# Performance work log

Measured on AMD Instinct MI355X. Metric: run time of the kernel, lower is better.

The kernel has to match this reference:

```python
import jax, jax.numpy as jnp
import numpy as np
import math

N_SRC = 100000
N_DST0 = 30000
N_DST1 = 8000
E0 = 200000
E1 = 80000
H, D = 4, 64


def gat_conv(h_src, h_dst, src, dst, W, al, ar, b, n_dst):
    """DGL GATConv (allow_zero_in_degree=True): shared fc, LeakyReLU(0.2), edge softmax."""
    z_src = (h_src @ W).reshape(-1, H, D)              # [Ns,H,D]
    z_dst = (h_dst @ W).reshape(-1, H, D)              # [Nd,H,D]
    el = jnp.sum(z_src * al, axis=-1)                  # [Ns,H]
    er = jnp.sum(z_dst * ar, axis=-1)                  # [Nd,H]
    e = jax.nn.leaky_relu(el[src] + er[dst], 0.2)      # [E,H]
    emax = jax.ops.segment_max(e, dst, num_segments=n_dst)
    emax = jnp.where(jnp.isfinite(emax), emax, 0.0)
    ex = jnp.exp(e - emax[dst])
    denom = jax.ops.segment_sum(ex, dst, num_segments=n_dst)
    denom = jnp.where(denom > 0, denom, 1.0)
    alpha = ex / denom[dst]                            # [E,H]
    out = jax.ops.segment_sum(alpha[:, :, None] * z_src[src], dst, num_segments=n_dst)
    return out + b.reshape(1, H, D)                    # [Nd,H,D]


def attn_pool(feat):
    """Self attention over relation/head slots, then mean over slots (attention(f,f,f).mean(dim=1))."""
    d = feat.shape[-1]
    scores = jnp.einsum('nsd,ntd->nst', feat, feat) / math.sqrt(d)
    p = jax.nn.softmax(scores, axis=-1)
    out = jnp.einsum('nst,ntd->nsd', p, feat)
    return out.mean(axis=1)                            # [N,d]


def rgat_layer(xu, xi, eii, eiu, eui, W, al, ar, b, n_dst_u, n_dst_i):
    du, di = xu[:n_dst_u], xi[:n_dst_i]
    # sorted canonical etypes: ('item','ii','item') < ('item','iu','user') < ('user','ui','item')
    out_ii = gat_conv(xi, di, eii[0], eii[1], W[0], al[0], ar[0], b[0], n_dst_i)
    out_iu = gat_conv(xi, du, eiu[0], eiu[1], W[1], al[1], ar[1], b[1], n_dst_u)
    out_ui = gat_conv(xu, di, eui[0], eui[1], W[2], al[2], ar[2], b[2], n_dst_i)
    feat_u = out_iu                                    # [Nu, H, D]
    feat_i = jnp.concatenate([out_ii, out_ui], axis=1) # [Ni, 2H, D]
    hu = attn_pool(feat_u)
    hi = attn_pool(feat_i)
    return jnp.concatenate([du, hu], axis=1), jnp.concatenate([di, hi], axis=1)


def setup_inputs() -> dict:
    key = jax.random.key(0)
    ks = jax.random.split(key, 24)
    inp = {
        'x_user': jax.random.normal(ks[0], (N_SRC, 64), jnp.float32),
        'x_item': jax.random.normal(ks[1], (N_SRC, 64), jnp.float32),
        'e0_ii_src': jax.random.randint(ks[2], (E0,), 0, N_SRC, jnp.int32),
        'e0_ii_dst': jax.random.randint(ks[3], (E0,), 0, N_DST0, jnp.int32),
        'e0_iu_src': jax.random.randint(ks[4], (E0,), 0, N_SRC, jnp.int32),
        'e0_iu_dst': jax.random.randint(ks[5], (E0,), 0, N_DST0, jnp.int32),
        'e0_ui_src': jax.random.randint(ks[6], (E0,), 0, N_SRC, jnp.int32),
        'e0_ui_dst': jax.random.randint(ks[7], (E0,), 0, N_DST0, jnp.int32),
        'e1_ii_src': jax.random.randint(ks[8], (E1,), 0, N_DST0, jnp.int32),
        'e1_ii_dst': jax.random.randint(ks[9], (E1,), 0, N_DST1, jnp.int32),
        'e1_iu_src': jax.random.randint(ks[10], (E1,), 0, N_DST0, jnp.int32),
        'e1_iu_dst': jax.random.randint(ks[11], (E1,), 0, N_DST1, jnp.int32),
        'e1_ui_src': jax.random.randint(ks[12], (E1,), 0, N_DST0, jnp.int32),
        'e1_ui_dst': jax.random.randint(ks[13], (E1,), 0, N_DST1, jnp.int32),
        'W0': jax.random.normal(ks[14], (3, 64, H * D), jnp.float32) * 0.1,
        'al0': jax.random.normal(ks[15], (3, H, D), jnp.float32) * 0.1,
        'ar0': jax.random.normal(ks[16], (3, H, D), jnp.float32) * 0.1,
        'b0': jnp.zeros((3, H * D), jnp.float32),
        'W1': jax.random.normal(ks[17], (3, 128, H * D), jnp.float32) * 0.1,
        'al1': jax.random.normal(ks[18], (3, H, D), jnp.float32) * 0.1,
        'ar1': jax.random.normal(ks[19], (3, H, D), jnp.float32) * 0.1,
        'b1': jnp.zeros((3, H * D), jnp.float32),
    }
    return inp


def reference(x_user, x_item,
              e0_ii_src, e0_ii_dst, e0_iu_src, e0_iu_dst, e0_ui_src, e0_ui_dst,
              e1_ii_src, e1_ii_dst, e1_iu_src, e1_iu_dst, e1_ui_src, e1_ui_dst,
              W0, al0, ar0, b0, W1, al1, ar1, b1):
    xu, xi = rgat_layer(x_user, x_item,
                        (e0_ii_src, e0_ii_dst), (e0_iu_src, e0_iu_dst), (e0_ui_src, e0_ui_dst),
                        W0, al0, ar0, b0, N_DST0, N_DST0)
    xu, xi = rgat_layer(xu, xi,
                        (e1_ii_src, e1_ii_dst), (e1_iu_src, e1_iu_dst), (e1_ui_src, e1_ui_dst),
                        W1, al1, ar1, b1, N_DST1, N_DST1)
    return jnp.concatenate([xu, xi], axis=0)  # [2*N_DST1, 128+64]
```

## Files before the change

### kernel.cpp

```cpp
#include <hip/hip_runtime.h>

#define NSRC   100000
#define NDST0  30000
#define NDST1  8000
#define E0N    200000
#define E1N    80000
#define HD     256
#define DD     64
#define CAPB   32

typedef short bf16x8 __attribute__((ext_vector_type(8)));
typedef float f32x4  __attribute__((ext_vector_type(4)));

static __device__ __forceinline__ unsigned short f2bf(float f) {
    unsigned u = __float_as_uint(f);
    u += 0x7fffu + ((u >> 16) & 1u);
    return (unsigned short)(u >> 16);
}
static __device__ __forceinline__ unsigned pack2(float a, float b) {
    return (unsigned)f2bf(a) | ((unsigned)f2bf(b) << 16);
}
static __device__ __forceinline__ void fma4(float4& a, float s, const float4& b) {
    a.x = fmaf(s, b.x, a.x); a.y = fmaf(s, b.y, a.y);
    a.z = fmaf(s, b.z, a.z); a.w = fmaf(s, b.w, a.w);
}
static __device__ __forceinline__ float dot4(const float4& a, const float4& b) {
    return fmaf(a.x, b.x, fmaf(a.y, b.y, fmaf(a.z, b.z, a.w * b.w)));
}
static __device__ __forceinline__ float4 ld_bf4(const unsigned short* p) {
    uint2 u = *reinterpret_cast<const uint2*>(p);
    float4 r;
    r.x = __uint_as_float(u.x << 16);
    r.y = __uint_as_float(u.x & 0xffff0000u);
    r.z = __uint_as_float(u.y << 16);
    r.w = __uint_as_float(u.y & 0xffff0000u);
    return r;
}

static __device__ void wlr_prep(const float* __restrict__ W, const float* __restrict__ al,
                                const float* __restrict__ ar, float* __restrict__ wl,
                                float* __restrict__ wr, int K, int tid)
{
    int r = tid / (K * 4);
    int rem = tid - r * K * 4;
    int k = rem >> 2, h = rem & 3;
    const float* wrow = W + (size_t)r * K * HD + (size_t)k * HD + h * DD;
    const float* a_l = al + r * HD + h * DD;
    const float* a_r = ar + r * HD + h * DD;
    float sl = 0.f, sr = 0.f;
    for (int d = 0; d < DD; ++d) {
        float w = wrow[d];
        sl = fmaf(w, a_l[d], sl);
        sr = fmaf(w, a_r[d], sr);
    }
    wl[r * 512 + k * 4 + h] = sl;
    wr[r * 512 + k * 4 + h] = sr;
}
static __device__ void wt_prep(const float* __restrict__ W, unsigned short* __restrict__ Wt,
                               int K, int r, int c)
{
    const float* Wr = W + (size_t)r * K * HD;
    unsigned short* Wtr = Wt + (size_t)r * 256 * K;
    for (int k = 0; k < K; k += 2) {
        float a = Wr[(size_t)k * HD + c];
        float b = Wr[(size_t)(k + 1) * HD + c];
        *reinterpret_cast<unsigned*>(Wtr + (size_t)c * K + k) = pack2(a, b);
    }
}
static __device__ void fill_aos(const int* __restrict__ ed, const int* __restrict__ es,
                                int* __restrict__ cnt, int* __restrict__ bsrc,
                                int E, int nd, int r, int e)
{
    if (e >= E) return;
    int d = __builtin_nontemporal_load(ed + e);
    int c = atomicAdd(&cnt[(size_t)r * nd + d], 1);
    if (c < CAPB) {
        int s = __builtin_nontemporal_load(es + e);
        __builtin_nontemporal_store(s, &bsrc[((size_t)r * nd + d) * CAPB + c]);
    }
}
template<int K>
static __device__ void prep_row(bool item, int row, int nd,
                                const float* __restrict__ XA, const float* __restrict__ XB,
                                const float* __restrict__ wl3, const float* __restrict__ wr3,
                                float* __restrict__ el3, float* __restrict__ er3)
{
    const float* X = item ? XA : XB;
    const float4* xv = reinterpret_cast<const float4*>(X + (size_t)row * K);
    const float4* wlAv = reinterpret_cast<const float4*>(item ? wl3 : wl3 + 1024);
    const float4* wlBv = reinterpret_cast<const float4*>(wl3 + 512);
    float4 aA = make_float4(0.f, 0.f, 0.f, 0.f), aB = aA;
    #pragma unroll 4
    for (int c = 0; c < K / 4; ++c) {
        float4 x4 = xv[c];
        fma4(aA, x4.x, wlAv[c * 4 + 0]); fma4(aA, x4.y, wlAv[c * 4 + 1]);
        fma4(aA, x4.z, wlAv[c * 4 + 2]); fma4(aA, x4.w, wlAv[c * 4 + 3]);
        if (item) {
            fma4(aB, x4.x, wlBv[c * 4 + 0]); fma4(aB, x4.y, wlBv[c * 4 + 1]);
            fma4(aB, x4.z, wlBv[c * 4 + 2]); fma4(aB, x4.w, wlBv[c * 4 + 3]);
        }
    }
    if (item) {
        *reinterpret_cast<float4*>(el3 + (size_t)row * 4) = aA;
        *reinterpret_cast<float4*>(el3 + (size_t)NSRC * 4 + (size_t)row * 4) = aB;
    } else {
        *reinterpret_cast<float4*>(el3 + (size_t)2 * NSRC * 4 + (size_t)row * 4) = aA;
    }
    if (row < nd) {
        const float4* wrAv = reinterpret_cast<const float4*>(item ? wr3 : wr3 + 512);
        const float4* wrBv = reinterpret_cast<const float4*>(wr3 + 1024);
        float4 rA = make_float4(0.f, 0.f, 0.f, 0.f), rB = rA;
        #pragma unroll 4
        for (int c = 0; c < K / 4; ++c) {
            float4 x4 = xv[c];
            fma4(rA, x4.x, wrAv[c * 4 + 0]); fma4(rA, x4.y, wrAv[c * 4 + 1]);
            fma4(rA, x4.z, wrAv[c * 4 + 2]); fma4(rA, x4.w, wrAv[c * 4 + 3]);
            if (item) {
                fma4(rB, x4.x, wrBv[c * 4 + 0]); fma4(rB, x4.y, wrBv[c * 4 + 1]);
                fma4(rB, x4.z, wrBv[c * 4 + 2]); fma4(rB, x4.w, wrBv[c * 4 + 3]);
            }
        }
        if (item) {
            *reinterpret_cast<float4*>(er3 + (size_t)row * 4) = rA;
            *reinterpret_cast<float4*>(er3 + (size_t)2 * NDST0 * 4 + (size_t)row * 4) = rB;
        } else {
            *reinterpret_cast<float4*>(er3 + (size_t)NDST0 * 4 + (size_t)row * 4) = rA;
        }
    }
}
template<int S>
static __device__ void pool_node(const unsigned short* __restrict__ srcA, const float* __restrict__ bA,
                                 const unsigned short* __restrict__ srcB, const float* __restrict__ bB,
                                 const float* __restrict__ base, int baseCols,
                                 float* __restrict__ dst, int pitch, int colOff,
                                 int node, int q)
{
    float4 f[S];
    #pragma unroll
    for (int s = 0; s < S; ++s) {
        const unsigned short* sp = (s < 4) ? (srcA + (size_t)node * HD + s * DD)
                                           : (srcB + (size_t)node * HD + (s - 4) * DD);
        const float* bp = (s < 4) ? (bA + s * DD) : (bB + (s - 4) * DD);
        float4 v = ld_bf4(sp + q * 4);
        float4 b = *reinterpret_cast<const float4*>(bp + q * 4);
        v.x += b.x; v.y += b.y; v.z += b.z; v.w += b.w;
        f[s] = v;
    }
    constexpr int NE = S * (S + 1) / 2;
    float gt[NE];
    {
        int idx = 0;
        #pragma unroll
        for (int s = 0; s < S; ++s)
            #pragma unroll
            for (int t = s; t < S; ++t)
                gt[idx++] = dot4(f[s], f[t]);
    }
    #pragma unroll
    for (int m = 1; m < 16; m <<= 1) {
        #pragma unroll
        for (int i = 0; i < NE; ++i) gt[i] += __shfl_xor(gt[i], m, 16);
    }
    auto Gv = [&](int s, int t) -> float {
        int a = s < t ? s : t, b2 = s < t ? t : s;
        return gt[a * S - a * (a - 1) / 2 + (b2 - a)];
    };
    float g[S];
    #pragma unroll
    for (int t = 0; t < S; ++t) g[t] = 0.f;
    #pragma unroll
    for (int s = 0; s < S; ++s) {
        float sc[S];
        float m = -1e30f;
        #pragma unroll
        for (int t = 0; t < S; ++t) { sc[t] = Gv(s, t) * 0.125f; m = sc[t] > m ? sc[t] : m; }
        float pe[S];
        float sum = 0.f;
        #pragma unroll
        for (int t = 0; t < S; ++t) { pe[t] = __expf(sc[t] - m); sum += pe[t]; }
        float inv = 1.f / sum;
        #pragma unroll
        for (int t = 0; t < S; ++t) g[t] += pe[t] * inv;
    }
    float4 o = make_float4(0.f, 0.f, 0.f, 0.f);
    #pragma unroll
    for (int t = 0; t < S; ++t) fma4(o, g[t], f[t]);
    const float is = 1.f / S;
    o.x *= is; o.y *= is; o.z *= is; o.w *= is;
    *reinterpret_cast<float4*>(dst + (size_t)node * pitch + colOff + q * 4) = o;
    for (int c = q * 4; c < baseCols; c += 64) {
        float4 v = *reinterpret_cast<const float4*>(base + (size_t)node * baseCols + c);
        *reinterpret_cast<float4*>(dst + (size_t)node * pitch + c) = v;
    }
}

__global__ void k_wsetup(const float* W0, const float* al0, const float* ar0,
                         const float* W1, const float* al1, const float* ar1,
                         float* wlA, float* wrA, unsigned short* WtA,
                         float* wlB, float* wrB, unsigned short* WtB,
                         int* cntA, int* cntB)
{
    int bx = blockIdx.x, t = threadIdx.x;
    if (bx < 3)       { wlr_prep(W0, al0, ar0, wlA, wrA, 64,  bx * 256 + t); return; }
    if (bx < 9)       { wlr_prep(W1, al1, ar1, wlB, wrB, 128, (bx - 3) * 256 + t); return; }
    if (bx < 12)      { wt_prep(W0, WtA, 64,  bx - 9,  t); return; }
    if (bx < 15)      { wt_prep(W1, WtB, 128, bx - 12, t); return; }
    bx -= 15;
    if (bx < 88) {
        int i = bx * 256 + t;
        if (i < 22500) reinterpret_cast<int4*>(cntA)[i] = make_int4(0, 0, 0, 0);
        return;
    }
    bx -= 88;
    {
        int i = bx * 256 + t;
        if (i < 6000) reinterpret_cast<int4*>(cntB)[i] = make_int4(0, 0, 0, 0);
    }
}

__global__ __launch_bounds__(256, 4) void k_prepfill(
    const float* x_item, const float* x_user,
    const float* wlA, const float* wrA,
    float* el3, float* er3,
    const int* ed0, const int* ed1, const int* ed2,
    const int* es0, const int* es1, const int* es2,
    const int* ed3, const int* ed4, const int* ed5,
    const int* es3, const int* es4, const int* es5,
    int* cntA, int* bsrcA, int* cntB, int* bsrcB,
    int bprP, int bpr0, int bpr1)
{
    int bx = blockIdx.x;
    int t = threadIdx.x;
    if (bx < 2 * bprP) {
        const bool item = bx < bprP;
        int row = (item ? bx : bx - bprP) * 256 + t;
        if (row < NSRC)
            prep_row<64>(item, row, NDST0, x_item, x_user, wlA, wrA, el3, er3);
        return;
    }
    bx -= 2 * bprP;
    if (bx < 3 * bpr0) {
        int r = (bx >= 2 * bpr0) ? 2 : (bx >= bpr0 ? 1 : 0);
        int e = (bx - r * bpr0) * 256 + t;
        const int* ed = (r == 0) ? ed0 : (r == 1 ? ed1 : ed2);
        const int* es = (r == 0) ? es0 : (r == 1 ? es1 : es2);
        fill_aos(ed, es, cntA, bsrcA, E0N, NDST0, r, e);
        return;
    }
    bx -= 3 * bpr0;
    {
        int r = (bx >= 2 * bpr1) ? 2 : (bx >= bpr1 ? 1 : 0);
        int e = (bx - r * bpr1) * 256 + t;
        const int* ed = (r == 0) ? ed3 : (r == 1 ? ed4 : ed5);
        const int* es = (r == 0) ? es3 : (r == 1 ? es4 : es5);
        fill_aos(ed, es, cntB, bsrcB, E1N, NDST1, r, e);
    }
}

template<int K>
__global__ __launch_bounds__(256) void k_prep_x2(const float* __restrict__ XA,
                                                 const float* __restrict__ XB,
                                                 int M, int nd, int bpr,
                                                 const float* __restrict__ wl3,
                                                 const float* __restrict__ wr3,
                                                 float* __restrict__ el3,
                                                 float* __restrict__ er3)
{
    int bx = blockIdx.x;
    const bool item = bx < bpr;
    int row = (item ? bx : bx - bpr) * 256 + threadIdx.x;
    if (row >= M) return;
    prep_row<K>(item, row, nd, XA, XB, wl3, wr3, el3, er3);
}

template<int K>
__global__ __launch_bounds__(256) void k_agg3(const int* __restrict__ cnt,
                                              const int* __restrict__ bsrc,
                                              const float* __restrict__ el3,
                                              const float* __restrict__ er3,
                                              const float* __restrict__ xsA,
                                              const float* __restrict__ xsB,
                                              unsigned short* __restrict__ aggX,
                                              int nd, int bpr)
{
    constexpr int NV = K / 64;
    __shared__ float exs[4][64][8];
    int bx = blockIdx.x;
    int r = (bx >= 2 * bpr) ? 2 : (bx >= bpr ? 1 : 0);
    int wid = ((bx - r * bpr) * 256 + (int)threadIdx.x) >> 6;
    int lane = threadIdx.x & 63;
    if (wid >= nd) return;
    int q = lane & 15, g = lane >> 4, w = threadIdx.x >> 6;
    const float* el = el3 + (size_t)r * NSRC * 4;
    const float* xsrc = (r < 2) ? xsA : xsB;
    int c = cnt[(size_t)r * nd + wid]; if (c > CAPB) c = CAPB;
    const int* lst = bsrc + ((size_t)r * nd + wid) * CAPB;
    float4 er4 = *reinterpret_cast<const float4*>(er3 + (size_t)r * NDST0 * 4 + (size_t)wid * 4);

    if (lane < c) {
        int s = lst[lane];
        float4 e4 = *reinterpret_cast<const float4*>(el + (size_t)s * 4);
        e4.x += er4.x; e4.y += er4.y; e4.z += er4.z; e4.w += er4.w;
        e4.x = e4.x > 0.f ? e4.x : 0.2f * e4.x;
        e4.y = e4.y > 0.f ? e4.y : 0.2f * e4.y;
        e4.z = e4.z > 0.f ? e4.z : 0.2f * e4.z;
        e4.w = e4.w > 0.f ? e4.w : 0.2f * e4.w;
        float sF = __int_as_float(s);
        float4 h0 = make_float4(sF, __expf(e4.x), sF, __expf(e4.y));
        float4 h1 = make_float4(sF, __expf(e4.z), sF, __expf(e4.w));
        *reinterpret_cast<float4*>(&exs[w][lane][0]) = h0;
        *reinterpret_cast<float4*>(&exs[w][lane][4]) = h1;
    }

    float4 acc[NV];
    #pragma unroll
    for (int v = 0; v < NV; ++v) acc[v] = make_float4(0.f, 0.f, 0.f, 0.f);
    float den = 0.f;
    const char* xb = reinterpret_cast<const char*>(xsrc) + q * (NV * 16);

    for (int b0 = 0; b0 < c; b0 += 4) {
        const int n = c - b0;
        float2 se0, se1, se2, se3;
        float4 x0[NV], x1[NV], x2[NV], x3[NV];
        se0 = *reinterpret_cast<const float2*>(&exs[w][b0][g * 2]);
        {
            const float4* xp = reinterpret_cast<const float4*>(
                xb + (size_t)((unsigned)__float_as_int(se0.x) * (K * 4)));
            #pragma unroll
            for (int v = 0; v < NV; ++v) x0[v] = xp[v];
        }
        if (n > 1) {
            se1 = *reinterpret_cast<const float2*>(&exs[w][b0 + 1][g * 2]);
            const float4* xp = reinterpret_cast<const float4*>(
                xb + (size_t)((unsigned)__float_as_int(se1.x) * (K * 4)));
            #pragma unroll
            for (int v = 0; v < NV; ++v) x1[v] = xp[v];
        }
        if (n > 2) {
            se2 = *reinterpret_cast<const float2*>(&exs[w][b0 + 2][g * 2]);
            const float4* xp = reinterpret_cast<const float4*>(
                xb + (size_t)((unsigned)__float_as_int(se2.x) * (K * 4)));
            #pragma unroll
            for (int v = 0; v < NV; ++v) x2[v] = xp[v];
        }
        if (n > 3) {
            se3 = *reinterpret_cast<const float2*>(&exs[w][b0 + 3][g * 2]);
            const float4* xp = reinterpret_cast<const float4*>(
                xb + (size_t)((unsigned)__float_as_int(se3.x) * (K * 4)));
            #pragma unroll
            for (int v = 0; v < NV; ++v) x3[v] = xp[v];
        }
        den += se0.y;
        #pragma unroll
        for (int v = 0; v < NV; ++v) fma4(acc[v], se0.y, x0[v]);
        if (n > 1) {
            den += se1.y;
            #pragma unroll
            for (int v = 0; v < NV; ++v) fma4(acc[v], se1.y, x1[v]);
        }
        if (n > 2) {
            den += se2.y;
            #pragma unroll
            for (int v = 0; v < NV; ++v) fma4(acc[v], se2.y, x2[v]);
        }
        if (n > 3) {
            den += se3.y;
            #pragma unroll
            for (int v = 0; v < NV; ++v) fma4(acc[v], se3.y, x3[v]);
        }
    }
    float inv = den > 0.f ? 1.f / den : 0.f;
    unsigned short* op = aggX + (((size_t)r * nd + wid) * 4 + g) * K + q * 4 * NV;
    if (NV == 1) {
        uint2 wv;
        wv.x = pack2(acc[0].x * inv, acc[0].y * inv);
        wv.y = pack2(acc[0].z * inv, acc[0].w * inv);
        *reinterpret_cast<uint2*>(op) = wv;
    } else {
        uint4 wv;
        wv.x = pack2(acc[0].x * inv, acc[0].y * inv);
        wv.y = pack2(acc[0].z * inv, acc[0].w * inv);
        wv.z = pack2(acc[1].x * inv, acc[1].y * inv);
        wv.w = pack2(acc[1].z * inv, acc[1].w * inv);
        *reinterpret_cast<uint4*>(op) = wv;
    }
}

template<int K>
__global__ __launch_bounds__(256) void k_gemm3(const unsigned short* __restrict__ aggX,
                                               const unsigned short* __restrict__ Wt3,
                                               unsigned short* __restrict__ outb,
                                               int nd, int bpr)
{
    int bx = blockIdx.x;
    int r = (bx >= 2 * bpr) ? 2 : (bx >= bpr ? 1 : 0);
    const unsigned short* A  = aggX + (size_t)r * nd * 4 * K;
    const unsigned short* Wt = Wt3 + (size_t)r * 256 * K;
    unsigned short* ob = outb + (size_t)r * NDST0 * HD;
    const int lane = threadIdx.x & 63;
    const int wv = threadIdx.x >> 6;
    const int r0 = (bx - r * bpr) * 16;
    const int rr = lane & 15, kg = lane >> 4;
    f32x4 acc[4] = {{0.f,0.f,0.f,0.f},{0.f,0.f,0.f,0.f},{0.f,0.f,0.f,0.f},{0.f,0.f,0.f,0.f}};
    const unsigned short* ap = A + ((size_t)(r0 + rr) * 4 + wv) * K + kg * 8;
    #pragma unroll
    for (int kb = 0; kb < K; kb += 32) {
        bf16x8 a = *reinterpret_cast<const bf16x8*>(ap + kb);
        #pragma unroll
        for (int n = 0; n < 4; ++n) {
            const unsigned short* wp = Wt + (size_t)(wv * 64 + n * 16 + rr) * K + kb + kg * 8;
            bf16x8 b = *reinterpret_cast<const bf16x8*>(wp);
            acc[n] = __builtin_amdgcn_mfma_f32_16x16x32_bf16(a, b, acc[n], 0, 0, 0);
        }
    }
    #pragma unroll
    for (int n = 0; n < 4; ++n)
        #pragma unroll
        for (int i = 0; i < 4; ++i)
            ob[(size_t)(r0 + kg * 4 + i) * HD + wv * 64 + n * 16 + rr] = f2bf(acc[n][i]);
}

__global__ __launch_bounds__(256) void k_pools(
    const unsigned short* pA4, const float* bA4, const unsigned short* pB4, const float* bB4,
    const float* base4, int cols4, float* dst4, int pitch4, int off4,
    const unsigned short* pA8, const float* bA8, const unsigned short* pB8, const float* bB8,
    const float* base8, int cols8, float* dst8, int pitch8, int off8,
    int n, int bp)
{
    int bx = blockIdx.x;
    int t = threadIdx.x;
    const bool four = bx < bp;
    int bl = four ? bx : bx - bp;
    int node = ((bl * 256 + t) >> 6) * 4 + ((t & 63) >> 4);
    int q = t & 15;
    if (node >= n) return;
    if (four) pool_node<4>(pA4, bA4, pB4, bB4, base4, cols4, dst4, pitch4, off4, node, q);
    else      pool_node<8>(pA8, bA8, pB8, bB8, base8, cols8, dst8, pitch8, off8, node, q);
}

extern "C" void kernel_launch(void* const* d_in, const int* in_sizes, int n_in,
                              void* d_out, int out_size, void* d_ws, size_t ws_size,
                              hipStream_t stream)
{
    const float* x_user = (const float*)d_in[0];
    const float* x_item = (const float*)d_in[1];
    const int* e_s[6] = { (const int*)d_in[2], (const int*)d_in[4], (const int*)d_in[6],
                          (const int*)d_in[8], (const int*)d_in[10], (const int*)d_in[12] };
    const int* e_d[6] = { (const int*)d_in[3], (const int*)d_in[5], (const int*)d_in[7],
                          (const int*)d_in[9], (const int*)d_in[11], (const int*)d_in[13] };
    const float* W0  = (const float*)d_in[14];
    const float* al0 = (const float*)d_in[15];
    const float* ar0 = (const float*)d_in[16];
    const float* b0  = (const float*)d_in[17];
    const float* W1  = (const float*)d_in[18];
    const float* al1 = (const float*)d_in[19];
    const float* ar1 = (const float*)d_in[20];
    const float* b1  = (const float*)d_in[21];
    float* out = (float*)d_out;
    (void)in_sizes; (void)n_in; (void)out_size; (void)ws_size;

    char* p = (char*)d_ws;
    auto take = [&](size_t bytes) { char* r = p; p += (bytes + 255) & ~(size_t)255; return r; };
    unsigned short* out3 = (unsigned short*)take((size_t)3 * NDST0 * HD * 2);
    float* xu1  = (float*)take((size_t)NDST0 * 128 * 4);
    float* xi1  = (float*)take((size_t)NDST0 * 128 * 4);
    unsigned short* aggX = (unsigned short*)take((size_t)3 * NDST0 * 4 * DD * 2);
    float* el3  = (float*)take((size_t)3 * NSRC * 4 * 4);
    float* er3  = (float*)take((size_t)3 * NDST0 * 4 * 4);
    int*   cntA = (int*)take((size_t)3 * NDST0 * 4);
    int*   cntB = (int*)take((size_t)3 * NDST1 * 4);
    int*   bsrcA = (int*)take((size_t)3 * NDST0 * CAPB * 4);
    int*   bsrcB = (int*)take((size_t)3 * NDST1 * CAPB * 4);
    unsigned short* WtA = (unsigned short*)take((size_t)3 * 256 * 64 * 2);
    unsigned short* WtB = (unsigned short*)take((size_t)3 * 256 * 128 * 2);
    float* wlA = (float*)take((size_t)3 * 512 * 4);
    float* wrA = (float*)take((size_t)3 * 512 * 4);
    float* wlB = (float*)take((size_t)3 * 512 * 4);
    float* wrB = (float*)take((size_t)3 * 512 * 4);

    unsigned short* out_ii = out3;
    unsigned short* out_iu = out3 + (size_t)NDST0 * HD;
    unsigned short* out_ui = out3 + (size_t)2 * NDST0 * HD;

    k_wsetup<<<15 + 88 + 24, 256, 0, stream>>>(W0, al0, ar0, W1, al1, ar1,
                                               wlA, wrA, WtA, wlB, wrB, WtB,
                                               cntA, cntB);
    const int bprP = (NSRC + 255) / 256;
    const int bpr0 = (E0N + 255) / 256;
    const int bpr1 = (E1N + 255) / 256;
    k_prepfill<<<2 * bprP + 3 * bpr0 + 3 * bpr1, 256, 0, stream>>>(
        x_item, x_user, wlA, wrA, el3, er3,
        e_d[0], e_d[1], e_d[2], e_s[0], e_s[1], e_s[2],
        e_d[3], e_d[4], e_d[5], e_s[3], e_s[4], e_s[5],
        cntA, bsrcA, cntB, bsrcB, bprP, bpr0, bpr1);

    {
        const int bprA = (NDST0 + 3) / 4;
        k_agg3<64><<<3 * bprA, 256, 0, stream>>>(cntA, bsrcA, el3, er3, x_item, x_user,
                                                 aggX, NDST0, bprA);
        const int bprG = NDST0 / 16;
        k_gemm3<64><<<3 * bprG, 256, 0, stream>>>(aggX, WtA, out3, NDST0, bprG);
        const int bp = NDST0 / 16;
        k_pools<<<2 * bp, 256, 0, stream>>>(
            out_iu, b0 + 256, out_iu, b0 + 256, x_user, 64, xu1, 128, 64,
            out_ii, b0,       out_ui, b0 + 512, x_item, 64, xi1, 128, 64,
            NDST0, bp);
    }

    {
        const int bprP2 = (NDST0 + 255) / 256;
        k_prep_x2<128><<<2 * bprP2, 256, 0, stream>>>(xi1, xu1, NDST0, NDST1, bprP2,
                                                      wlB, wrB, el3, er3);
        const int bprA = (NDST1 + 3) / 4;
        k_agg3<128><<<3 * bprA, 256, 0, stream>>>(cntB, bsrcB, el3, er3, xi1, xu1,
                                                  aggX, NDST1, bprA);
        const int bprG = NDST1 / 16;
        k_gemm3<128><<<3 * bprG, 256, 0, stream>>>(aggX, WtB, out3, NDST1, bprG);
        const int bp = NDST1 / 16;
        k_pools<<<2 * bp, 256, 0, stream>>>(
            out_iu, b1 + 256, out_iu, b1 + 256, xu1, 128, out, 192, 128,
            out_ii, b1,       out_ui, b1 + 512, xi1, 128, out + (size_t)NDST1 * 192, 192, 128,
            NDST1, bp);
    }
}
```

Before: 293.5 us.

## Fuse per-relation GEMM with attention pooling via LDS staging

Merges the three-relation projection GEMM and the attention-pool kernel into one kernel. Each block computes all three relations' outputs for 16 destination nodes, stages them as bf16 in shared memory, then pools user and item features directly. This removes the global out3 intermediate round-trip and one launch per layer. It also drops the nontemporal hints in the edge-bucket fill. The cost is a larger per-block workload and fewer blocks for the GEMM, since relations are now serialized inside one block.

New measurement: 279.9 us. 4.6% less time.

```diff
diff --git a/kernel.cpp b/kernel.cpp
--- a/kernel.cpp
+++ b/kernel.cpp
@@ -8,6 +8,7 @@
 #define HD     256
 #define DD     64
 #define CAPB   32
+#define LROW   776
 
 typedef short bf16x8 __attribute__((ext_vector_type(8)));
 typedef float f32x4  __attribute__((ext_vector_type(4)));
@@ -72,12 +73,9 @@
                                 int E, int nd, int r, int e)
 {
     if (e >= E) return;
-    int d = __builtin_nontemporal_load(ed + e);
+    int d = ed[e];
     int c = atomicAdd(&cnt[(size_t)r * nd + d], 1);
-    if (c < CAPB) {
-        int s = __builtin_nontemporal_load(es + e);
-        __builtin_nontemporal_store(s, &bsrc[((size_t)r * nd + d) * CAPB + c]);
-    }
+    if (c < CAPB) bsrc[((size_t)r * nd + d) * CAPB + c] = es[e];
 }
 template<int K>
 static __device__ void prep_row(bool item, int row, int nd,
@@ -129,19 +127,19 @@
     }
 }
 template<int S>
-static __device__ void pool_node(const unsigned short* __restrict__ srcA, const float* __restrict__ bA,
-                                 const unsigned short* __restrict__ srcB, const float* __restrict__ bB,
-                                 const float* __restrict__ base, int baseCols,
-                                 float* __restrict__ dst, int pitch, int colOff,
-                                 int node, int q)
+static __device__ void pool_node_lds(const unsigned short* __restrict__ ldsRow,
+                                     int colA, const float* __restrict__ bA,
+                                     int colB, const float* __restrict__ bB,
+                                     const float* __restrict__ base, int baseCols,
+                                     float* __restrict__ dst, int pitch, int colOff,
+                                     int node, int q)
 {
     float4 f[S];
     #pragma unroll
     for (int s = 0; s < S; ++s) {
-        const unsigned short* sp = (s < 4) ? (srcA + (size_t)node * HD + s * DD)
-                                           : (srcB + (size_t)node * HD + (s - 4) * DD);
+        int col = (s < 4) ? (colA + s * DD) : (colB + (s - 4) * DD);
         const float* bp = (s < 4) ? (bA + s * DD) : (bB + (s - 4) * DD);
-        float4 v = ld_bf4(sp + q * 4);
+        float4 v = ld_bf4(ldsRow + col + q * 4);
         float4 b = *reinterpret_cast<const float4*>(bp + q * 4);
         v.x += b.x; v.y += b.y; v.z += b.z; v.w += b.w;
         f[s] = v;
@@ -387,55 +385,49 @@
 }
 
 template<int K>
-__global__ __launch_bounds__(256) void k_gemm3(const unsigned short* __restrict__ aggX,
-                                               const unsigned short* __restrict__ Wt3,
-                                               unsigned short* __restrict__ outb,
-                                               int nd, int bpr)
-{
-    int bx = blockIdx.x;
-    int r = (bx >= 2 * bpr) ? 2 : (bx >= bpr ? 1 : 0);
-    const unsigned short* A  = aggX + (size_t)r * nd * 4 * K;
-    const unsigned short* Wt = Wt3 + (size_t)r * 256 * K;
-    unsigned short* ob = outb + (size_t)r * NDST0 * HD;
+__global__ __launch_bounds__(256) void k_gemmpool(
+    const unsigned short* __restrict__ aggX, const unsigned short* __restrict__ Wt3,
+    int nd, const float* __restrict__ bias,
+    const float* __restrict__ baseU, int colsU, float* __restrict__ dstU, int pitchU, int offU,
+    const float* __restrict__ baseI, int colsI, float* __restrict__ dstI, int pitchI, int offI)
+{
+    __shared__ unsigned short ldsOut[16][LROW];
+    const int d0 = blockIdx.x * 16;
     const int lane = threadIdx.x & 63;
     const int wv = threadIdx.x >> 6;
-    const int r0 = (bx - r * bpr) * 16;
     const int rr = lane & 15, kg = lane >> 4;
-    f32x4 acc[4] = {{0.f,0.f,0.f,0.f},{0.f,0.f,0.f,0.f},{0.f,0.f,0.f,0.f},{0.f,0.f,0.f,0.f}};
-    const unsigned short* ap = A + ((size_t)(r0 + rr) * 4 + wv) * K + kg * 8;
-    #pragma unroll
-    for (int kb = 0; kb < K; kb += 32) {
-        bf16x8 a = *reinterpret_cast<const bf16x8*>(ap + kb);
-        #pragma unroll
-        for (int n = 0; n < 4; ++n) {
-            const unsigned short* wp = Wt + (size_t)(wv * 64 + n * 16 + rr) * K + kb + kg * 8;
-            bf16x8 b = *reinterpret_cast<const bf16x8*>(wp);
-            acc[n] = __builtin_amdgcn_mfma_f32_16x16x32_bf16(a, b, acc[n], 0, 0, 0);
-        }
-    }
-    #pragma unroll
-    for (int n = 0; n < 4; ++n)
-        #pragma unroll
-        for (int i = 0; i < 4; ++i)
-            ob[(size_t)(r0 + kg * 4 + i) * HD + wv * 64 + n * 16 + rr] = f2bf(acc[n][i]);
-}
-
-__global__ __launch_bounds__(256) void k_pools(
-    const unsigned short* pA4, const float* bA4, const unsigned short* pB4, const float* bB4,
-    const float* base4, int cols4, float* dst4, int pitch4, int off4,
-    const unsigned short* pA8, const float* bA8, const unsigned short* pB8, const float* bB8,
-    const float* base8, int cols8, float* dst8, int pitch8, int off8,
-    int n, int bp)
-{
-    int bx = blockIdx.x;
-    int t = threadIdx.x;
-    const bool four = bx < bp;
-    int bl = four ? bx : bx - bp;
-    int node = ((bl * 256 + t) >> 6) * 4 + ((t & 63) >> 4);
-    int q = t & 15;
-    if (node >= n) return;
-    if (four) pool_node<4>(pA4, bA4, pB4, bB4, base4, cols4, dst4, pitch4, off4, node, q);
-    else      pool_node<8>(pA8, bA8, pB8, bB8, base8, cols8, dst8, pitch8, off8, node, q);
+
+    #pragma unroll
+    for (int r = 0; r < 3; ++r) {
+        const unsigned short* A  = aggX + (size_t)r * nd * 4 * K;
+        const unsigned short* Wt = Wt3 + (size_t)r * 256 * K;
+        f32x4 acc[4] = {{0.f,0.f,0.f,0.f},{0.f,0.f,0.f,0.f},{0.f,0.f,0.f,0.f},{0.f,0.f,0.f,0.f}};
+        const unsigned short* ap = A + ((size_t)(d0 + rr) * 4 + wv) * K + kg * 8;
+        #pragma unroll
+        for (int kb = 0; kb < K; kb += 32) {
+            bf16x8 a = *reinterpret_cast<const bf16x8*>(ap + kb);
+            #pragma unroll
+            for (int n = 0; n < 4; ++n) {
+                const unsigned short* wp = Wt + (size_t)(wv * 64 + n * 16 + rr) * K + kb + kg * 8;
+                bf16x8 b = *reinterpret_cast<const bf16x8*>(wp);
+                acc[n] = __builtin_amdgcn_mfma_f32_16x16x32_bf16(a, b, acc[n], 0, 0, 0);
+            }
+        }
+        #pragma unroll
+        for (int n = 0; n < 4; ++n)
+            #pragma unroll
+            for (int i = 0; i < 4; ++i)
+                ldsOut[kg * 4 + i][r * 256 + wv * 64 + n * 16 + rr] = f2bf(acc[n][i]);
+    }
+    __syncthreads();
+
+    const int nl = wv * 4 + (lane >> 4);
+    const int q = lane & 15;
+    const int node = d0 + nl;
+    pool_node_lds<4>(ldsOut[nl], 256, bias + 256, 256, bias + 256,
+                     baseU, colsU, dstU, pitchU, offU, node, q);
+    pool_node_lds<8>(ldsOut[nl], 0, bias, 512, bias + 512,
+                     baseI, colsI, dstI, pitchI, offI, node, q);
 }
 
 extern "C" void kernel_launch(void* const* d_in, const int* in_sizes, int n_in,
@@ -461,7 +453,6 @@
 
     char* p = (char*)d_ws;
     auto take = [&](size_t bytes) { char* r = p; p += (bytes + 255) & ~(size_t)255; return r; };
-    unsigned short* out3 = (unsigned short*)take((size_t)3 * NDST0 * HD * 2);
     float* xu1  = (float*)take((size_t)NDST0 * 128 * 4);
     float* xi1  = (float*)take((size_t)NDST0 * 128 * 4);
     unsigned short* aggX = (unsigned short*)take((size_t)3 * NDST0 * 4 * DD * 2);
@@ -478,10 +469,6 @@
     float* wlB = (float*)take((size_t)3 * 512 * 4);
     float* wrB = (float*)take((size_t)3 * 512 * 4);
 
-    unsigned short* out_ii = out3;
-    unsigned short* out_iu = out3 + (size_t)NDST0 * HD;
-    unsigned short* out_ui = out3 + (size_t)2 * NDST0 * HD;
-
     k_wsetup<<<15 + 88 + 24, 256, 0, stream>>>(W0, al0, ar0, W1, al1, ar1,
                                                wlA, wrA, WtA, wlB, wrB, WtB,
                                                cntA, cntB);
@@ -498,13 +485,10 @@
         const int bprA = (NDST0 + 3) / 4;
         k_agg3<64><<<3 * bprA, 256, 0, stream>>>(cntA, bsrcA, el3, er3, x_item, x_user,
                                                  aggX, NDST0, bprA);
-        const int bprG = NDST0 / 16;
-        k_gemm3<64><<<3 * bprG, 256, 0, stream>>>(aggX, WtA, out3, NDST0, bprG);
-        const int bp = NDST0 / 16;
-        k_pools<<<2 * bp, 256, 0, stream>>>(
-            out_iu, b0 + 256, out_iu, b0 + 256, x_user, 64, xu1, 128, 64,
-            out_ii, b0,       out_ui, b0 + 512, x_item, 64, xi1, 128, 64,
-            NDST0, bp);
+        k_gemmpool<64><<<NDST0 / 16, 256, 0, stream>>>(
+            aggX, WtA, NDST0, b0,
+            x_user, 64, xu1, 128, 64,
+            x_item, 64, xi1, 128, 64);
     }
 
     {
@@ -514,12 +498,9 @@
         const int bprA = (NDST1 + 3) / 4;
         k_agg3<128><<<3 * bprA, 256, 0, stream>>>(cntB, bsrcB, el3, er3, xi1, xu1,
                                                   aggX, NDST1, bprA);
-        const int bprG = NDST1 / 16;
-        k_gemm3<128><<<3 * bprG, 256, 0, stream>>>(aggX, WtB, out3, NDST1, bprG);
-        const int bp = NDST1 / 16;
-        k_pools<<<2 * bp, 256, 0, stream>>>(
-            out_iu, b1 + 256, out_iu, b1 + 256, xu1, 128, out, 192, 128,
-            out_ii, b1,       out_ui, b1 + 512, xi1, 128, out + (size_t)NDST1 * 192, 192, 128,
-            NDST1, bp);
-    }
-}
+        k_gemmpool<128><<<NDST1 / 16, 256, 0, stream>>>(
+            aggX, WtB, NDST1, b1,
+            xu1, 128, out, 192, 128,
+            xi1, 128, out + (size_t)NDST1 * 192, 192, 128);
+    }
+}
```
